# Optimization experiments

Hardware: AMD Instinct MI355X
Metric: run time of the kernel (lower is better)

## Reference

```python
import jax, jax.numpy as jnp
import numpy as np
from jax import lax

B, Q, T, G = 128, 900, 256, 20
FOCAL_ALPHA, FOCAL_GAMMA = 0.25, 2.0
COEF_BBOX, COEF_GIOU, COEF_CLASS = 5.0, 2.0, 1.0
EPS = 1e-6


def setup_inputs() -> dict:
    key = jax.random.key(0)
    k1, k2, k3, k4, k5 = jax.random.split(key, 5)
    pred_logits = jax.random.normal(k1, (B, Q, T), dtype=jnp.float32)
    # pred boxes in cxcywh, valid-ish: centers in (0.2,0.8), w/h in (0.05,0.3)
    cxy_p = jax.random.uniform(k2, (B, Q, 2), minval=0.2, maxval=0.8)
    wh_p = jax.random.uniform(k3, (B, Q, 2), minval=0.05, maxval=0.3)
    pred_boxes = jnp.concatenate([cxy_p, wh_p], axis=-1).astype(jnp.float32)
    cxy_t = jax.random.uniform(k4, (B, G, 2), minval=0.2, maxval=0.8)
    wh_t = jax.random.uniform(k5, (B, G, 2), minval=0.05, maxval=0.3)
    tgt_boxes = jnp.concatenate([cxy_t, wh_t], axis=-1).astype(jnp.float32)
    ks, kl = jax.random.split(jax.random.fold_in(key, 7))
    start = jax.random.randint(ks, (B, G, 1), 0, T - 6)
    length = jax.random.randint(kl, (B, G, 1), 1, 6)
    tokens_positive = jnp.concatenate([start, start + length], axis=-1).astype(jnp.int32)
    return {"pred_logits": pred_logits, "pred_boxes": pred_boxes,
            "tgt_boxes": tgt_boxes, "tokens_positive": tokens_positive}


def cxcywh_to_xyxy(b):
    cx, cy, w, h = b[..., 0], b[..., 1], b[..., 2], b[..., 3]
    return jnp.stack([cx - 0.5 * w, cy - 0.5 * h, cx + 0.5 * w, cy + 0.5 * h], axis=-1)


def box_iou_pairwise(b1, b2):
    # b1: [Q,4], b2: [G,4] xyxy -> iou [Q,G]
    a1 = (b1[:, 2] - b1[:, 0]) * (b1[:, 3] - b1[:, 1])
    a2 = (b2[:, 2] - b2[:, 0]) * (b2[:, 3] - b2[:, 1])
    lt = jnp.maximum(b1[:, None, :2], b2[None, :, :2])
    rb = jnp.minimum(b1[:, None, 2:], b2[None, :, 2:])
    wh = jnp.clip(rb - lt, 0.0)
    inter = wh[..., 0] * wh[..., 1]
    union = a1[:, None] + a2[None, :] - inter
    return inter / union


def giou_elementwise(b1, b2):
    # b1, b2: [G,4] xyxy (matched pairs) -> giou [G]
    a1 = (b1[:, 2] - b1[:, 0]) * (b1[:, 3] - b1[:, 1])
    a2 = (b2[:, 2] - b2[:, 0]) * (b2[:, 3] - b2[:, 1])
    lt = jnp.maximum(b1[:, :2], b2[:, :2])
    rb = jnp.minimum(b1[:, 2:], b2[:, 2:])
    wh = jnp.clip(rb - lt, 0.0)
    inter = wh[:, 0] * wh[:, 1]
    union = a1 + a2 - inter
    iou = inter / union
    lt_c = jnp.minimum(b1[:, :2], b2[:, :2])
    rb_c = jnp.maximum(b1[:, 2:], b2[:, 2:])
    wh_c = jnp.clip(rb_c - lt_c, 0.0)
    area_c = wh_c[:, 0] * wh_c[:, 1]
    return iou - (area_c - union) / area_c


def ensure_valid_boxes(b):
    x1, y1, x2, y2 = b[:, 0], b[:, 1], b[:, 2], b[:, 3]
    x2v = jnp.maximum(x2, x1 + EPS)
    y2v = jnp.maximum(y2, y1 + EPS)
    return jnp.clip(jnp.stack([x1, y1, x2v, y2v], axis=-1), 0.0, 1.0)


def sigmoid_focal_loss(logits, targets):
    p = jax.nn.sigmoid(logits)
    ce = jnp.maximum(logits, 0.0) - logits * targets + jnp.log1p(jnp.exp(-jnp.abs(logits)))
    p_t = p * targets + (1.0 - p) * (1.0 - targets)
    loss = ce * (1.0 - p_t) ** FOCAL_GAMMA
    alpha_t = FOCAL_ALPHA * targets + (1.0 - FOCAL_ALPHA) * (1.0 - targets)
    return (alpha_t * loss).mean()


def _per_batch(pred_boxes_b, pred_logits_b, tgt_boxes_b, spans_b):
    pred_xyxy = cxcywh_to_xyxy(pred_boxes_b)          # [Q,4]
    tgt_xyxy = cxcywh_to_xyxy(tgt_boxes_b)            # [G,4]
    iou = lax.stop_gradient(box_iou_pairwise(pred_xyxy, tgt_xyxy))  # [Q,G]

    # greedy sequential matching: for each gt column, argmax over remaining preds
    def step(mat, g):
        best = jnp.argmax(mat[:, g])
        mat = mat.at[best].set(-1.0)
        return mat, best
    _, matched = lax.scan(step, iou, jnp.arange(G))   # [G] pred indices

    matched_boxes = pred_boxes_b[matched]             # [G,4]
    loss_bbox = jnp.sum(jnp.abs(matched_boxes - tgt_boxes_b))

    matched_xyxy = ensure_valid_boxes(cxcywh_to_xyxy(matched_boxes))
    tgt_valid = ensure_valid_boxes(tgt_xyxy)
    giou = giou_elementwise(matched_xyxy, tgt_valid)
    loss_giou = jnp.sum(1.0 - giou)

    # target_classes [Q,T]: rows at matched indices get 1 over the gt token span
    pos = jnp.arange(T)
    span_mask = ((pos[None, :] >= spans_b[:, 0:1]) & (pos[None, :] < spans_b[:, 1:2])).astype(jnp.float32)  # [G,T]
    target_classes = jnp.zeros((Q, T), dtype=jnp.float32).at[matched].max(span_mask)

    loss_class = sigmoid_focal_loss(pred_logits_b, target_classes)
    return loss_bbox, loss_giou, loss_class


def reference(pred_logits, pred_boxes, tgt_boxes, tokens_positive):
    lb, lg, lc = jax.vmap(_per_batch)(pred_boxes, pred_logits, tgt_boxes, tokens_positive)
    num_boxes = jnp.float32(B * G)
    loss_bbox = COEF_BBOX * jnp.sum(lb) / num_boxes
    loss_giou = COEF_GIOU * jnp.sum(lg) / num_boxes
    loss_class = COEF_CLASS * jnp.sum(lc) / num_boxes
    loss_total = loss_bbox + loss_giou + loss_class
    return jnp.stack([loss_bbox, loss_giou, loss_class, loss_total])
```

## Files before the change

### kernel.cpp

```cpp
#include <hip/hip_runtime.h>
#include <hip/hip_bf16.h>

#define NB 128
#define NQ 900
#define NT 256
#define NG 20
#define NR 15
#define FOCAL_BLOCKS 1800
#define MATCH_BLOCKS 128
#define TOTAL_BLOCKS (FOCAL_BLOCKS + MATCH_BLOCKS)
#define FWAVES (FOCAL_BLOCKS * 4)

#define WS_BB 7200
#define WS_GI 7328
#define WS_DL 7456

__device__ __forceinline__ float clamp01(float v) {
    return fminf(fmaxf(v, 0.0f), 1.0f);
}

__device__ __forceinline__ float focal_neg_term(float x) {
    float ax  = fabsf(x);
    float em  = __expf(-ax);
    float a1  = 1.0f + em;
    float ce  = fmaxf(x, 0.0f) + __logf(a1);
    float inv = __builtin_amdgcn_rcpf(a1);
    float p   = (x >= 0.0f) ? inv : em * inv;
    return ce * p * p;
}

__device__ __forceinline__ float focal_delta_term(float x) {
    float ax     = fabsf(x);
    float em     = __expf(-ax);
    float a1     = 1.0f + em;
    float lg     = __logf(a1);
    float ce0    = fmaxf(x, 0.0f) + lg;
    float ce1    = ce0 - x;
    float inv    = __builtin_amdgcn_rcpf(a1);
    float em_inv = em * inv;
    float p      = (x >= 0.0f) ? inv : em_inv;
    float omp    = (x >= 0.0f) ? em_inv : inv;
    return 0.25f * ce1 * omp * omp - 0.75f * ce0 * p * p;
}

__device__ __forceinline__ float focal_row_sum4(float4 v) {
    return focal_neg_term(v.x) + focal_neg_term(v.y) +
           focal_neg_term(v.z) + focal_neg_term(v.w);
}

__global__ __launch_bounds__(256) void main_kernel(
    const float4* __restrict__ logits,
    const float4* __restrict__ pred_boxes,
    const float4* __restrict__ tgt_boxes,
    const int2*   __restrict__ tokens,
    float*        __restrict__ ws)
{
    if (blockIdx.x >= MATCH_BLOCKS) {
        const int lane = threadIdx.x & 63;
        const int gw   = ((blockIdx.x - MATCH_BLOCKS) * 256 + threadIdx.x) >> 6;

        float sum = 0.0f;
        #pragma unroll
        for (int i = 0; i < 2; ++i) {
            int row0 = (gw + i * FWAVES) * 8;
            const float4* base = logits + (size_t)row0 * (NT / 4) + lane;
            float4 v0 = base[0 * (NT / 4)];
            float4 v1 = base[1 * (NT / 4)];
            float4 v2 = base[2 * (NT / 4)];
            float4 v3 = base[3 * (NT / 4)];
            float4 v4 = base[4 * (NT / 4)];
            float4 v5 = base[5 * (NT / 4)];
            float4 v6 = base[6 * (NT / 4)];
            float4 v7 = base[7 * (NT / 4)];
            sum += focal_row_sum4(v0) + focal_row_sum4(v1) +
                   focal_row_sum4(v2) + focal_row_sum4(v3) +
                   focal_row_sum4(v4) + focal_row_sum4(v5) +
                   focal_row_sum4(v6) + focal_row_sum4(v7);
        }
        #pragma unroll
        for (int off = 32; off > 0; off >>= 1) sum += __shfl_down(sum, off);
        if (lane == 0) ws[gw] = sum;
        return;
    }

    if (threadIdx.x >= 64) return;
    const int b    = blockIdx.x;
    const int lane = threadIdx.x;

    float px1[NR], py1[NR], px2[NR], py2[NR], pa[NR];
    int avail = 0;
    #pragma unroll
    for (int r = 0; r < NR; ++r) {
        int q = lane + 64 * r;
        if (q < NQ) {
            float4 pb = pred_boxes[b * NQ + q];
            px1[r] = pb.x - 0.5f * pb.z; py1[r] = pb.y - 0.5f * pb.w;
            px2[r] = pb.x + 0.5f * pb.z; py2[r] = pb.y + 0.5f * pb.w;
            pa[r]  = (px2[r] - px1[r]) * (py2[r] - py1[r]);
            avail |= (1 << r);
        } else {
            px1[r] = 0.0f; py1[r] = 0.0f; px2[r] = 0.0f; py2[r] = 0.0f;
            pa[r] = 0.0f;
        }
    }

    int my_q = 0;
    for (int g = 0; g < NG; ++g) {
        float4 tb = tgt_boxes[b * NG + g];
        float gx1 = tb.x - 0.5f * tb.z, gy1 = tb.y - 0.5f * tb.w;
        float gx2 = tb.x + 0.5f * tb.z, gy2 = tb.y + 0.5f * tb.w;
        float ga  = (gx2 - gx1) * (gy2 - gy1);
        float bv = -2.0f;
        int   bi = 0x7fffffff;
        #pragma unroll
        for (int r = 0; r < NR; ++r) {
            float ix1 = fmaxf(px1[r], gx1), iy1 = fmaxf(py1[r], gy1);
            float ix2 = fminf(px2[r], gx2), iy2 = fminf(py2[r], gy2);
            float iw = fmaxf(ix2 - ix1, 0.0f), ih = fmaxf(iy2 - iy1, 0.0f);
            float inter = iw * ih;
            float v = inter / (pa[r] + ga - inter);
            bool ok = (avail >> r) & 1;
            v = ok ? v : -1.0f;
            int q = lane + 64 * r;
            if (v > bv) { bv = v; bi = q; }
        }
        #pragma unroll
        for (int off = 1; off < 64; off <<= 1) {
            float ov = __shfl_xor(bv, off);
            int   oi = __shfl_xor(bi, off);
            if (ov > bv || (ov == bv && oi < bi)) { bv = ov; bi = oi; }
        }
        if (lane == g) my_q = bi;
        if ((bi & 63) == lane) avail &= ~(1 << (bi >> 6));
    }

    float lb = 0.0f, lgi = 0.0f, dl = 0.0f;
    if (lane < NG) {
        int g = lane, q = my_q;
        float4 pb = pred_boxes[b * NQ + q];
        float4 tb = tgt_boxes[b * NG + g];
        lb = fabsf(pb.x - tb.x) + fabsf(pb.y - tb.y) +
             fabsf(pb.z - tb.z) + fabsf(pb.w - tb.w);

        float mx1 = pb.x - 0.5f * pb.z, my1 = pb.y - 0.5f * pb.w;
        float mx2 = pb.x + 0.5f * pb.z, my2 = pb.y + 0.5f * pb.w;
        mx2 = fmaxf(mx2, mx1 + 1e-6f);  my2 = fmaxf(my2, my1 + 1e-6f);
        mx1 = clamp01(mx1); my1 = clamp01(my1);
        mx2 = clamp01(mx2); my2 = clamp01(my2);

        float gx1 = tb.x - 0.5f * tb.z, gy1 = tb.y - 0.5f * tb.w;
        float gx2 = tb.x + 0.5f * tb.z, gy2 = tb.y + 0.5f * tb.w;
        gx2 = fmaxf(gx2, gx1 + 1e-6f);  gy2 = fmaxf(gy2, gy1 + 1e-6f);
        gx1 = clamp01(gx1); gy1 = clamp01(gy1);
        gx2 = clamp01(gx2); gy2 = clamp01(gy2);

        float a1 = (mx2 - mx1) * (my2 - my1);
        float a2 = (gx2 - gx1) * (gy2 - gy1);
        float ix1 = fmaxf(mx1, gx1), iy1 = fmaxf(my1, gy1);
        float ix2 = fminf(mx2, gx2), iy2 = fminf(my2, gy2);
        float iw = fmaxf(ix2 - ix1, 0.0f), ih = fmaxf(iy2 - iy1, 0.0f);
        float inter = iw * ih;
        float uni   = a1 + a2 - inter;
        float iou   = inter / uni;
        float cx1 = fminf(mx1, gx1), cy1 = fminf(my1, gy1);
        float cx2 = fmaxf(mx2, gx2), cy2 = fmaxf(my2, gy2);
        float ac  = fmaxf(cx2 - cx1, 0.0f) * fmaxf(cy2 - cy1, 0.0f);
        lgi = 1.0f - (iou - (ac - uni) / ac);

        int2 tk = tokens[b * NG + g];
        const float* rowp = (const float*)logits + (size_t)(b * NQ + q) * NT;
        for (int t = tk.x; t < tk.y; ++t) dl += focal_delta_term(rowp[t]);
    }
    #pragma unroll
    for (int off = 32; off > 0; off >>= 1) {
        lb  += __shfl_down(lb,  off);
        lgi += __shfl_down(lgi, off);
        dl  += __shfl_down(dl,  off);
    }
    if (lane == 0) {
        ws[WS_BB + b] = lb;
        ws[WS_GI + b] = lgi;
        ws[WS_DL + b] = dl;
    }
}

__global__ __launch_bounds__(256) void finalize_kernel(
    const float* __restrict__ ws, float* __restrict__ out)
{
    const int tid  = threadIdx.x;
    const int lane = tid & 63;
    const int wav  = tid >> 6;

    float s_neg = 0.0f;
    for (int i = tid; i < FWAVES; i += 256) s_neg += ws[i];
    float s_bb = 0.0f, s_gi = 0.0f, s_dl = 0.0f;
    if (tid < NB) {
        s_bb = ws[WS_BB + tid];
        s_gi = ws[WS_GI + tid];
        s_dl = ws[WS_DL + tid];
    }
    #pragma unroll
    for (int off = 32; off > 0; off >>= 1) {
        s_neg += __shfl_down(s_neg, off);
        s_bb  += __shfl_down(s_bb,  off);
        s_gi  += __shfl_down(s_gi,  off);
        s_dl  += __shfl_down(s_dl,  off);
    }
    __shared__ float red[4][4];
    if (lane == 0) {
        red[0][wav] = s_neg; red[1][wav] = s_bb;
        red[2][wav] = s_gi;  red[3][wav] = s_dl;
    }
    __syncthreads();
    if (tid == 0) {
        float neg = red[0][0] + red[0][1] + red[0][2] + red[0][3];
        float bb  = red[1][0] + red[1][1] + red[1][2] + red[1][3];
        float gi  = red[2][0] + red[2][1] + red[2][2] + red[2][3];
        float dlt = red[3][0] + red[3][1] + red[3][2] + red[3][3];
        const float num_boxes = (float)(NB * NG);
        float lb = 5.0f * bb / num_boxes;
        float lg = 2.0f * gi / num_boxes;
        float cls_sum = 0.75f * neg + dlt;
        float lc = (cls_sum / (float)(NQ * NT)) / num_boxes;
        out[0] = lb;
        out[1] = lg;
        out[2] = lc;
        out[3] = lb + lg + lc;
    }
}

extern "C" void kernel_launch(void* const* d_in, const int* in_sizes, int n_in,
                              void* d_out, int out_size, void* d_ws, size_t ws_size,
                              hipStream_t stream) {
    const float4* pred_logits4 = (const float4*)d_in[0];
    const float4* pred_boxes4  = (const float4*)d_in[1];
    const float4* tgt_boxes4   = (const float4*)d_in[2];
    const int2*   tokens2      = (const int2*)d_in[3];

    float* ws = (float*)d_ws;

    main_kernel<<<TOTAL_BLOCKS, 256, 0, stream>>>(pred_logits4, pred_boxes4,
                                                  tgt_boxes4, tokens2, ws);
    finalize_kernel<<<1, 256, 0, stream>>>(ws, (float*)d_out);
}
```

Before: 192.1 us.

## Fuse finalize into cooperative grid-synced kernel and shrink focal grid

Replaces the two-kernel launch with one cooperative kernel that does the partial work, a grid-wide sync, and the final reduction in block 0. The focal grid drops to 960 blocks so the grid can stay resident, and the focal loop becomes grid-stride. The matcher now stages pred boxes and areas in shared memory instead of 75 registers per lane. This removes the second launch and its gap, at the price of a grid barrier, fewer waves in flight for the memory-bound focal pass, and shared-memory reads in the matching inner loop. If the cooperative launch fails, it falls back to the old two-kernel path.

```diff
diff --git a/kernel.cpp b/kernel.cpp
--- a/kernel.cpp
+++ b/kernel.cpp
@@ -1,22 +1,33 @@
 #include <hip/hip_runtime.h>
 #include <hip/hip_bf16.h>
+#include <hip/hip_cooperative_groups.h>
+
+namespace cg = cooperative_groups;
 
 #define NB 128
 #define NQ 900
 #define NT 256
 #define NG 20
 #define NR 15
-#define FOCAL_BLOCKS 1800
+#define FOCAL_BLOCKS 832
 #define MATCH_BLOCKS 128
 #define TOTAL_BLOCKS (FOCAL_BLOCKS + MATCH_BLOCKS)
 #define FWAVES (FOCAL_BLOCKS * 4)
-
-#define WS_BB 7200
-#define WS_GI 7328
-#define WS_DL 7456
+#define NCHUNK 14400
+
+#define WS_BB 3328
+#define WS_GI 3456
+#define WS_DL 3584
 
 __device__ __forceinline__ float clamp01(float v) {
     return fminf(fmaxf(v, 0.0f), 1.0f);
+}
+
+__device__ __forceinline__ void ws_store(float* p, float v) {
+    __hip_atomic_store(p, v, __ATOMIC_RELAXED, __HIP_MEMORY_SCOPE_AGENT);
+}
+__device__ __forceinline__ float ws_load(const float* p) {
+    return __hip_atomic_load(p, __ATOMIC_RELAXED, __HIP_MEMORY_SCOPE_AGENT);
 }
 
 __device__ __forceinline__ float focal_neg_term(float x) {
@@ -48,61 +59,53 @@
            focal_neg_term(v.z) + focal_neg_term(v.w);
 }
 
-__global__ __launch_bounds__(256) void main_kernel(
-    const float4* __restrict__ logits,
-    const float4* __restrict__ pred_boxes,
-    const float4* __restrict__ tgt_boxes,
-    const int2*   __restrict__ tokens,
-    float*        __restrict__ ws)
-{
-    if (blockIdx.x >= MATCH_BLOCKS) {
-        const int lane = threadIdx.x & 63;
-        const int gw   = ((blockIdx.x - MATCH_BLOCKS) * 256 + threadIdx.x) >> 6;
-
-        float sum = 0.0f;
-        #pragma unroll
-        for (int i = 0; i < 2; ++i) {
-            int row0 = (gw + i * FWAVES) * 8;
-            const float4* base = logits + (size_t)row0 * (NT / 4) + lane;
-            float4 v0 = base[0 * (NT / 4)];
-            float4 v1 = base[1 * (NT / 4)];
-            float4 v2 = base[2 * (NT / 4)];
-            float4 v3 = base[3 * (NT / 4)];
-            float4 v4 = base[4 * (NT / 4)];
-            float4 v5 = base[5 * (NT / 4)];
-            float4 v6 = base[6 * (NT / 4)];
-            float4 v7 = base[7 * (NT / 4)];
-            sum += focal_row_sum4(v0) + focal_row_sum4(v1) +
-                   focal_row_sum4(v2) + focal_row_sum4(v3) +
-                   focal_row_sum4(v4) + focal_row_sum4(v5) +
-                   focal_row_sum4(v6) + focal_row_sum4(v7);
-        }
-        #pragma unroll
-        for (int off = 32; off > 0; off >>= 1) sum += __shfl_down(sum, off);
-        if (lane == 0) ws[gw] = sum;
-        return;
-    }
+__device__ void focal_path(const float4* __restrict__ logits,
+                           float* __restrict__ ws, int fblock) {
+    const int lane = threadIdx.x & 63;
+    const int gw   = (fblock * 256 + (int)threadIdx.x) >> 6;
+
+    float sum = 0.0f;
+    for (int c = gw; c < NCHUNK; c += FWAVES) {
+        const float4* base = logits + (size_t)(c * 8) * (NT / 4) + lane;
+        float4 v0 = base[0 * (NT / 4)];
+        float4 v1 = base[1 * (NT / 4)];
+        float4 v2 = base[2 * (NT / 4)];
+        float4 v3 = base[3 * (NT / 4)];
+        float4 v4 = base[4 * (NT / 4)];
+        float4 v5 = base[5 * (NT / 4)];
+        float4 v6 = base[6 * (NT / 4)];
+        float4 v7 = base[7 * (NT / 4)];
+        sum += focal_row_sum4(v0) + focal_row_sum4(v1) +
+               focal_row_sum4(v2) + focal_row_sum4(v3) +
+               focal_row_sum4(v4) + focal_row_sum4(v5) +
+               focal_row_sum4(v6) + focal_row_sum4(v7);
+    }
+    #pragma unroll
+    for (int off = 32; off > 0; off >>= 1) sum += __shfl_down(sum, off);
+    if (lane == 0) ws_store(&ws[gw], sum);
+}
+
+__device__ void match_path(const float4* __restrict__ logits,
+                           const float4* __restrict__ pred_boxes,
+                           const float4* __restrict__ tgt_boxes,
+                           const int2*   __restrict__ tokens,
+                           float* __restrict__ ws,
+                           float4* sbox, float* sarea, int b) {
+    for (int q = threadIdx.x; q < NQ; q += 256) {
+        float4 pb = pred_boxes[b * NQ + q];
+        float x1 = pb.x - 0.5f * pb.z, y1 = pb.y - 0.5f * pb.w;
+        float x2 = pb.x + 0.5f * pb.z, y2 = pb.y + 0.5f * pb.w;
+        sbox[q]  = make_float4(x1, y1, x2, y2);
+        sarea[q] = (x2 - x1) * (y2 - y1);
+    }
+    __syncthreads();
 
     if (threadIdx.x >= 64) return;
-    const int b    = blockIdx.x;
     const int lane = threadIdx.x;
-
-    float px1[NR], py1[NR], px2[NR], py2[NR], pa[NR];
-    int avail = 0;
+    int avail = (1 << NR) - 1;
     #pragma unroll
-    for (int r = 0; r < NR; ++r) {
-        int q = lane + 64 * r;
-        if (q < NQ) {
-            float4 pb = pred_boxes[b * NQ + q];
-            px1[r] = pb.x - 0.5f * pb.z; py1[r] = pb.y - 0.5f * pb.w;
-            px2[r] = pb.x + 0.5f * pb.z; py2[r] = pb.y + 0.5f * pb.w;
-            pa[r]  = (px2[r] - px1[r]) * (py2[r] - py1[r]);
-            avail |= (1 << r);
-        } else {
-            px1[r] = 0.0f; py1[r] = 0.0f; px2[r] = 0.0f; py2[r] = 0.0f;
-            pa[r] = 0.0f;
-        }
-    }
+    for (int r = 0; r < NR; ++r)
+        if (lane + 64 * r >= NQ) avail &= ~(1 << r);
 
     int my_q = 0;
     for (int g = 0; g < NG; ++g) {
@@ -114,14 +117,17 @@
         int   bi = 0x7fffffff;
         #pragma unroll
         for (int r = 0; r < NR; ++r) {
-            float ix1 = fmaxf(px1[r], gx1), iy1 = fmaxf(py1[r], gy1);
-            float ix2 = fminf(px2[r], gx2), iy2 = fminf(py2[r], gy2);
+            int q = lane + 64 * r;
+            bool ok = (avail >> r) & 1;
+            int qs = ok ? q : 0;
+            float4 pbx = sbox[qs];
+            float pa   = sarea[qs];
+            float ix1 = fmaxf(pbx.x, gx1), iy1 = fmaxf(pbx.y, gy1);
+            float ix2 = fminf(pbx.z, gx2), iy2 = fminf(pbx.w, gy2);
             float iw = fmaxf(ix2 - ix1, 0.0f), ih = fmaxf(iy2 - iy1, 0.0f);
             float inter = iw * ih;
-            float v = inter / (pa[r] + ga - inter);
-            bool ok = (avail >> r) & 1;
+            float v = inter / (pa + ga - inter);
             v = ok ? v : -1.0f;
-            int q = lane + 64 * r;
             if (v > bv) { bv = v; bi = q; }
         }
         #pragma unroll
@@ -178,26 +184,25 @@
         dl  += __shfl_down(dl,  off);
     }
     if (lane == 0) {
-        ws[WS_BB + b] = lb;
-        ws[WS_GI + b] = lgi;
-        ws[WS_DL + b] = dl;
-    }
-}
-
-__global__ __launch_bounds__(256) void finalize_kernel(
-    const float* __restrict__ ws, float* __restrict__ out)
-{
+        ws_store(&ws[WS_BB + b], lb);
+        ws_store(&ws[WS_GI + b], lgi);
+        ws_store(&ws[WS_DL + b], dl);
+    }
+}
+
+__device__ void finalize_body(const float* __restrict__ ws,
+                              float* __restrict__ out) {
     const int tid  = threadIdx.x;
     const int lane = tid & 63;
     const int wav  = tid >> 6;
 
     float s_neg = 0.0f;
-    for (int i = tid; i < FWAVES; i += 256) s_neg += ws[i];
+    for (int i = tid; i < FWAVES; i += 256) s_neg += ws_load(&ws[i]);
     float s_bb = 0.0f, s_gi = 0.0f, s_dl = 0.0f;
     if (tid < NB) {
-        s_bb = ws[WS_BB + tid];
-        s_gi = ws[WS_GI + tid];
-        s_dl = ws[WS_DL + tid];
+        s_bb = ws_load(&ws[WS_BB + tid]);
+        s_gi = ws_load(&ws[WS_GI + tid]);
+        s_dl = ws_load(&ws[WS_DL + tid]);
     }
     #pragma unroll
     for (int off = 32; off > 0; off >>= 1) {
@@ -229,6 +234,55 @@
     }
 }
 
+__global__ __launch_bounds__(256, 4) void coop_kernel(
+    const float4* __restrict__ logits,
+    const float4* __restrict__ pred_boxes,
+    const float4* __restrict__ tgt_boxes,
+    const int2*   __restrict__ tokens,
+    float*        __restrict__ ws,
+    float*        __restrict__ out)
+{
+    __shared__ float4 sbox[NQ];
+    __shared__ float  sarea[NQ];
+
+    if (blockIdx.x >= MATCH_BLOCKS) {
+        focal_path(logits, ws, blockIdx.x - MATCH_BLOCKS);
+    } else {
+        match_path(logits, pred_boxes, tgt_boxes, tokens, ws, sbox, sarea,
+                   blockIdx.x);
+    }
+
+    __threadfence();
+    cg::this_grid().sync();
+    __threadfence();
+
+    if (blockIdx.x == 0) finalize_body(ws, out);
+}
+
+__global__ __launch_bounds__(256, 4) void partials_kernel(
+    const float4* __restrict__ logits,
+    const float4* __restrict__ pred_boxes,
+    const float4* __restrict__ tgt_boxes,
+    const int2*   __restrict__ tokens,
+    float*        __restrict__ ws)
+{
+    __shared__ float4 sbox[NQ];
+    __shared__ float  sarea[NQ];
+
+    if (blockIdx.x >= MATCH_BLOCKS) {
+        focal_path(logits, ws, blockIdx.x - MATCH_BLOCKS);
+    } else {
+        match_path(logits, pred_boxes, tgt_boxes, tokens, ws, sbox, sarea,
+                   blockIdx.x);
+    }
+}
+
+__global__ __launch_bounds__(256) void finalize_kernel(
+    const float* __restrict__ ws, float* __restrict__ out)
+{
+    finalize_body(ws, out);
+}
+
 extern "C" void kernel_launch(void* const* d_in, const int* in_sizes, int n_in,
                               void* d_out, int out_size, void* d_ws, size_t ws_size,
                               hipStream_t stream) {
@@ -236,10 +290,19 @@
     const float4* pred_boxes4  = (const float4*)d_in[1];
     const float4* tgt_boxes4   = (const float4*)d_in[2];
     const int2*   tokens2      = (const int2*)d_in[3];
-
-    float* ws = (float*)d_ws;
-
-    main_kernel<<<TOTAL_BLOCKS, 256, 0, stream>>>(pred_logits4, pred_boxes4,
-                                                  tgt_boxes4, tokens2, ws);
-    finalize_kernel<<<1, 256, 0, stream>>>(ws, (float*)d_out);
-}
+    float*        ws           = (float*)d_ws;
+    float*        outp         = (float*)d_out;
+
+    void* args[] = { (void*)&pred_logits4, (void*)&pred_boxes4,
+                     (void*)&tgt_boxes4,   (void*)&tokens2,
+                     (void*)&ws,           (void*)&outp };
+    hipError_t err = hipLaunchCooperativeKernel((const void*)coop_kernel,
+                                                dim3(TOTAL_BLOCKS), dim3(256),
+                                                args, 0, stream);
+    if (err != hipSuccess) {
+        (void)hipGetLastError();
+        partials_kernel<<<TOTAL_BLOCKS, 256, 0, stream>>>(
+            pred_logits4, pred_boxes4, tgt_boxes4, tokens2, ws);
+        finalize_kernel<<<1, 256, 0, stream>>>(ws, outp);
+    }
+}
```

Measured after the change: 482.9 us. 151% more time.

## Fuse finalize reduction into main kernel via last-block ticket counter

Applied to the files above, without the earlier changes.

Removes the separate finalize launch. Each block now increments an atomic ticket in the workspace after its partial results. The block that sees the final count performs the global reduction and resets the ticket. The focal-loss loop also changes from two iterations of 8 rows to four iterations of 4 rows per wave, which alters load batching. The ticket logic assumes the workspace starts at a fixed poison value (0xAAAAAAAA), so correctness on the first call depends on how the harness initialises the workspace.

```diff
diff --git a/kernel.cpp b/kernel.cpp
--- a/kernel.cpp
+++ b/kernel.cpp
@@ -14,9 +14,18 @@
 #define WS_BB 7200
 #define WS_GI 7328
 #define WS_DL 7456
+#define WS_TICKET 7584
+#define TICKET_INIT 0xAAAAAAAAu
 
 __device__ __forceinline__ float clamp01(float v) {
     return fminf(fmaxf(v, 0.0f), 1.0f);
+}
+
+__device__ __forceinline__ void ws_store(float* p, float v) {
+    __hip_atomic_store(p, v, __ATOMIC_RELAXED, __HIP_MEMORY_SCOPE_AGENT);
+}
+__device__ __forceinline__ float ws_load(const float* p) {
+    return __hip_atomic_load(p, __ATOMIC_RELAXED, __HIP_MEMORY_SCOPE_AGENT);
 }
 
 __device__ __forceinline__ float focal_neg_term(float x) {
@@ -53,179 +62,186 @@
     const float4* __restrict__ pred_boxes,
     const float4* __restrict__ tgt_boxes,
     const int2*   __restrict__ tokens,
-    float*        __restrict__ ws)
+    float*        __restrict__ ws,
+    float*        __restrict__ out)
 {
     if (blockIdx.x >= MATCH_BLOCKS) {
         const int lane = threadIdx.x & 63;
-        const int gw   = ((blockIdx.x - MATCH_BLOCKS) * 256 + threadIdx.x) >> 6;
+        const int gw   = ((blockIdx.x - MATCH_BLOCKS) * 256 + (int)threadIdx.x) >> 6;
 
         float sum = 0.0f;
         #pragma unroll
-        for (int i = 0; i < 2; ++i) {
-            int row0 = (gw + i * FWAVES) * 8;
+        for (int i = 0; i < 4; ++i) {
+            int row0 = (gw + i * FWAVES) * 4;
             const float4* base = logits + (size_t)row0 * (NT / 4) + lane;
             float4 v0 = base[0 * (NT / 4)];
             float4 v1 = base[1 * (NT / 4)];
             float4 v2 = base[2 * (NT / 4)];
             float4 v3 = base[3 * (NT / 4)];
-            float4 v4 = base[4 * (NT / 4)];
-            float4 v5 = base[5 * (NT / 4)];
-            float4 v6 = base[6 * (NT / 4)];
-            float4 v7 = base[7 * (NT / 4)];
             sum += focal_row_sum4(v0) + focal_row_sum4(v1) +
-                   focal_row_sum4(v2) + focal_row_sum4(v3) +
-                   focal_row_sum4(v4) + focal_row_sum4(v5) +
-                   focal_row_sum4(v6) + focal_row_sum4(v7);
+                   focal_row_sum4(v2) + focal_row_sum4(v3);
         }
         #pragma unroll
         for (int off = 32; off > 0; off >>= 1) sum += __shfl_down(sum, off);
-        if (lane == 0) ws[gw] = sum;
-        return;
-    }
-
-    if (threadIdx.x >= 64) return;
-    const int b    = blockIdx.x;
-    const int lane = threadIdx.x;
-
-    float px1[NR], py1[NR], px2[NR], py2[NR], pa[NR];
-    int avail = 0;
-    #pragma unroll
-    for (int r = 0; r < NR; ++r) {
-        int q = lane + 64 * r;
-        if (q < NQ) {
+        if (lane == 0) ws_store(&ws[gw], sum);
+    } else if (threadIdx.x < 64) {
+        const int b    = blockIdx.x;
+        const int lane = threadIdx.x;
+
+        float px1[NR], py1[NR], px2[NR], py2[NR], pa[NR];
+        int avail = 0;
+        #pragma unroll
+        for (int r = 0; r < NR; ++r) {
+            int q = lane + 64 * r;
+            if (q < NQ) {
+                float4 pb = pred_boxes[b * NQ + q];
+                px1[r] = pb.x - 0.5f * pb.z; py1[r] = pb.y - 0.5f * pb.w;
+                px2[r] = pb.x + 0.5f * pb.z; py2[r] = pb.y + 0.5f * pb.w;
+                pa[r]  = (px2[r] - px1[r]) * (py2[r] - py1[r]);
+                avail |= (1 << r);
+            } else {
+                px1[r] = 0.0f; py1[r] = 0.0f; px2[r] = 0.0f; py2[r] = 0.0f;
+                pa[r] = 0.0f;
+            }
+        }
+
+        int my_q = 0;
+        for (int g = 0; g < NG; ++g) {
+            float4 tb = tgt_boxes[b * NG + g];
+            float gx1 = tb.x - 0.5f * tb.z, gy1 = tb.y - 0.5f * tb.w;
+            float gx2 = tb.x + 0.5f * tb.z, gy2 = tb.y + 0.5f * tb.w;
+            float ga  = (gx2 - gx1) * (gy2 - gy1);
+            float bv = -2.0f;
+            int   bi = 0x7fffffff;
+            #pragma unroll
+            for (int r = 0; r < NR; ++r) {
+                float ix1 = fmaxf(px1[r], gx1), iy1 = fmaxf(py1[r], gy1);
+                float ix2 = fminf(px2[r], gx2), iy2 = fminf(py2[r], gy2);
+                float iw = fmaxf(ix2 - ix1, 0.0f), ih = fmaxf(iy2 - iy1, 0.0f);
+                float inter = iw * ih;
+                float v = inter / (pa[r] + ga - inter);
+                bool ok = (avail >> r) & 1;
+                v = ok ? v : -1.0f;
+                int q = lane + 64 * r;
+                if (v > bv) { bv = v; bi = q; }
+            }
+            #pragma unroll
+            for (int off = 1; off < 64; off <<= 1) {
+                float ov = __shfl_xor(bv, off);
+                int   oi = __shfl_xor(bi, off);
+                if (ov > bv || (ov == bv && oi < bi)) { bv = ov; bi = oi; }
+            }
+            if (lane == g) my_q = bi;
+            if ((bi & 63) == lane) avail &= ~(1 << (bi >> 6));
+        }
+
+        float lb = 0.0f, lgi = 0.0f, dl = 0.0f;
+        if (lane < NG) {
+            int g = lane, q = my_q;
             float4 pb = pred_boxes[b * NQ + q];
-            px1[r] = pb.x - 0.5f * pb.z; py1[r] = pb.y - 0.5f * pb.w;
-            px2[r] = pb.x + 0.5f * pb.z; py2[r] = pb.y + 0.5f * pb.w;
-            pa[r]  = (px2[r] - px1[r]) * (py2[r] - py1[r]);
-            avail |= (1 << r);
-        } else {
-            px1[r] = 0.0f; py1[r] = 0.0f; px2[r] = 0.0f; py2[r] = 0.0f;
-            pa[r] = 0.0f;
-        }
-    }
-
-    int my_q = 0;
-    for (int g = 0; g < NG; ++g) {
-        float4 tb = tgt_boxes[b * NG + g];
-        float gx1 = tb.x - 0.5f * tb.z, gy1 = tb.y - 0.5f * tb.w;
-        float gx2 = tb.x + 0.5f * tb.z, gy2 = tb.y + 0.5f * tb.w;
-        float ga  = (gx2 - gx1) * (gy2 - gy1);
-        float bv = -2.0f;
-        int   bi = 0x7fffffff;
-        #pragma unroll
-        for (int r = 0; r < NR; ++r) {
-            float ix1 = fmaxf(px1[r], gx1), iy1 = fmaxf(py1[r], gy1);
-            float ix2 = fminf(px2[r], gx2), iy2 = fminf(py2[r], gy2);
+            float4 tb = tgt_boxes[b * NG + g];
+            lb = fabsf(pb.x - tb.x) + fabsf(pb.y - tb.y) +
+                 fabsf(pb.z - tb.z) + fabsf(pb.w - tb.w);
+
+            float mx1 = pb.x - 0.5f * pb.z, my1 = pb.y - 0.5f * pb.w;
+            float mx2 = pb.x + 0.5f * pb.z, my2 = pb.y + 0.5f * pb.w;
+            mx2 = fmaxf(mx2, mx1 + 1e-6f);  my2 = fmaxf(my2, my1 + 1e-6f);
+            mx1 = clamp01(mx1); my1 = clamp01(my1);
+            mx2 = clamp01(mx2); my2 = clamp01(my2);
+
+            float gx1 = tb.x - 0.5f * tb.z, gy1 = tb.y - 0.5f * tb.w;
+            float gx2 = tb.x + 0.5f * tb.z, gy2 = tb.y + 0.5f * tb.w;
+            gx2 = fmaxf(gx2, gx1 + 1e-6f);  gy2 = fmaxf(gy2, gy1 + 1e-6f);
+            gx1 = clamp01(gx1); gy1 = clamp01(gy1);
+            gx2 = clamp01(gx2); gy2 = clamp01(gy2);
+
+            float a1 = (mx2 - mx1) * (my2 - my1);
+            float a2 = (gx2 - gx1) * (gy2 - gy1);
+            float ix1 = fmaxf(mx1, gx1), iy1 = fmaxf(my1, gy1);
+            float ix2 = fminf(mx2, gx2), iy2 = fminf(my2, gy2);
             float iw = fmaxf(ix2 - ix1, 0.0f), ih = fmaxf(iy2 - iy1, 0.0f);
             float inter = iw * ih;
-            float v = inter / (pa[r] + ga - inter);
-            bool ok = (avail >> r) & 1;
-            v = ok ? v : -1.0f;
-            int q = lane + 64 * r;
-            if (v > bv) { bv = v; bi = q; }
-        }
-        #pragma unroll
-        for (int off = 1; off < 64; off <<= 1) {
-            float ov = __shfl_xor(bv, off);
-            int   oi = __shfl_xor(bi, off);
-            if (ov > bv || (ov == bv && oi < bi)) { bv = ov; bi = oi; }
-        }
-        if (lane == g) my_q = bi;
-        if ((bi & 63) == lane) avail &= ~(1 << (bi >> 6));
+            float uni   = a1 + a2 - inter;
+            float iou   = inter / uni;
+            float cx1 = fminf(mx1, gx1), cy1 = fminf(my1, gy1);
+            float cx2 = fmaxf(mx2, gx2), cy2 = fmaxf(my2, gy2);
+            float ac  = fmaxf(cx2 - cx1, 0.0f) * fmaxf(cy2 - cy1, 0.0f);
+            lgi = 1.0f - (iou - (ac - uni) / ac);
+
+            int2 tk = tokens[b * NG + g];
+            const float* rowp = (const float*)logits + (size_t)(b * NQ + q) * NT;
+            for (int t = tk.x; t < tk.y; ++t) dl += focal_delta_term(rowp[t]);
+        }
+        #pragma unroll
+        for (int off = 32; off > 0; off >>= 1) {
+            lb  += __shfl_down(lb,  off);
+            lgi += __shfl_down(lgi, off);
+            dl  += __shfl_down(dl,  off);
+        }
+        if (lane == 0) {
+            ws_store(&ws[WS_BB + b], lb);
+            ws_store(&ws[WS_GI + b], lgi);
+            ws_store(&ws[WS_DL + b], dl);
+        }
     }
 
-    float lb = 0.0f, lgi = 0.0f, dl = 0.0f;
-    if (lane < NG) {
-        int g = lane, q = my_q;
-        float4 pb = pred_boxes[b * NQ + q];
-        float4 tb = tgt_boxes[b * NG + g];
-        lb = fabsf(pb.x - tb.x) + fabsf(pb.y - tb.y) +
-             fabsf(pb.z - tb.z) + fabsf(pb.w - tb.w);
-
-        float mx1 = pb.x - 0.5f * pb.z, my1 = pb.y - 0.5f * pb.w;
-        float mx2 = pb.x + 0.5f * pb.z, my2 = pb.y + 0.5f * pb.w;
-        mx2 = fmaxf(mx2, mx1 + 1e-6f);  my2 = fmaxf(my2, my1 + 1e-6f);
-        mx1 = clamp01(mx1); my1 = clamp01(my1);
-        mx2 = clamp01(mx2); my2 = clamp01(my2);
-
-        float gx1 = tb.x - 0.5f * tb.z, gy1 = tb.y - 0.5f * tb.w;
-        float gx2 = tb.x + 0.5f * tb.z, gy2 = tb.y + 0.5f * tb.w;
-        gx2 = fmaxf(gx2, gx1 + 1e-6f);  gy2 = fmaxf(gy2, gy1 + 1e-6f);
-        gx1 = clamp01(gx1); gy1 = clamp01(gy1);
-        gx2 = clamp01(gx2); gy2 = clamp01(gy2);
-
-        float a1 = (mx2 - mx1) * (my2 - my1);
-        float a2 = (gx2 - gx1) * (gy2 - gy1);
-        float ix1 = fmaxf(mx1, gx1), iy1 = fmaxf(my1, gy1);
-        float ix2 = fminf(mx2, gx2), iy2 = fminf(my2, gy2);
-        float iw = fmaxf(ix2 - ix1, 0.0f), ih = fmaxf(iy2 - iy1, 0.0f);
-        float inter = iw * ih;
-        float uni   = a1 + a2 - inter;
-        float iou   = inter / uni;
-        float cx1 = fminf(mx1, gx1), cy1 = fminf(my1, gy1);
-        float cx2 = fmaxf(mx2, gx2), cy2 = fmaxf(my2, gy2);
-        float ac  = fmaxf(cx2 - cx1, 0.0f) * fmaxf(cy2 - cy1, 0.0f);
-        lgi = 1.0f - (iou - (ac - uni) / ac);
-
-        int2 tk = tokens[b * NG + g];
-        const float* rowp = (const float*)logits + (size_t)(b * NQ + q) * NT;
-        for (int t = tk.x; t < tk.y; ++t) dl += focal_delta_term(rowp[t]);
-    }
-    #pragma unroll
-    for (int off = 32; off > 0; off >>= 1) {
-        lb  += __shfl_down(lb,  off);
-        lgi += __shfl_down(lgi, off);
-        dl  += __shfl_down(dl,  off);
-    }
-    if (lane == 0) {
-        ws[WS_BB + b] = lb;
-        ws[WS_GI + b] = lgi;
-        ws[WS_DL + b] = dl;
-    }
-}
-
-__global__ __launch_bounds__(256) void finalize_kernel(
-    const float* __restrict__ ws, float* __restrict__ out)
-{
-    const int tid  = threadIdx.x;
-    const int lane = tid & 63;
-    const int wav  = tid >> 6;
-
-    float s_neg = 0.0f;
-    for (int i = tid; i < FWAVES; i += 256) s_neg += ws[i];
-    float s_bb = 0.0f, s_gi = 0.0f, s_dl = 0.0f;
-    if (tid < NB) {
-        s_bb = ws[WS_BB + tid];
-        s_gi = ws[WS_GI + tid];
-        s_dl = ws[WS_DL + tid];
-    }
-    #pragma unroll
-    for (int off = 32; off > 0; off >>= 1) {
-        s_neg += __shfl_down(s_neg, off);
-        s_bb  += __shfl_down(s_bb,  off);
-        s_gi  += __shfl_down(s_gi,  off);
-        s_dl  += __shfl_down(s_dl,  off);
-    }
-    __shared__ float red[4][4];
-    if (lane == 0) {
-        red[0][wav] = s_neg; red[1][wav] = s_bb;
-        red[2][wav] = s_gi;  red[3][wav] = s_dl;
+    __shared__ bool lastFlag;
+    unsigned int* ticket = (unsigned int*)&ws[WS_TICKET];
+
+    __threadfence();
+    __syncthreads();
+    if (threadIdx.x == 0) {
+        unsigned int old = __hip_atomic_fetch_add(
+            ticket, 1u, __ATOMIC_ACQ_REL, __HIP_MEMORY_SCOPE_AGENT);
+        lastFlag = (old == TICKET_INIT + (unsigned)(TOTAL_BLOCKS - 1));
     }
     __syncthreads();
-    if (tid == 0) {
-        float neg = red[0][0] + red[0][1] + red[0][2] + red[0][3];
-        float bb  = red[1][0] + red[1][1] + red[1][2] + red[1][3];
-        float gi  = red[2][0] + red[2][1] + red[2][2] + red[2][3];
-        float dlt = red[3][0] + red[3][1] + red[3][2] + red[3][3];
-        const float num_boxes = (float)(NB * NG);
-        float lb = 5.0f * bb / num_boxes;
-        float lg = 2.0f * gi / num_boxes;
-        float cls_sum = 0.75f * neg + dlt;
-        float lc = (cls_sum / (float)(NQ * NT)) / num_boxes;
-        out[0] = lb;
-        out[1] = lg;
-        out[2] = lc;
-        out[3] = lb + lg + lc;
+    if (!lastFlag) return;
+
+    __threadfence();
+    {
+        const int tid  = threadIdx.x;
+        const int lane = tid & 63;
+        const int wav  = tid >> 6;
+
+        float s_neg = 0.0f;
+        for (int i = tid; i < FWAVES; i += 256) s_neg += ws_load(&ws[i]);
+        float s_bb = 0.0f, s_gi = 0.0f, s_dl = 0.0f;
+        if (tid < NB) {
+            s_bb = ws_load(&ws[WS_BB + tid]);
+            s_gi = ws_load(&ws[WS_GI + tid]);
+            s_dl = ws_load(&ws[WS_DL + tid]);
+        }
+        #pragma unroll
+        for (int off = 32; off > 0; off >>= 1) {
+            s_neg += __shfl_down(s_neg, off);
+            s_bb  += __shfl_down(s_bb,  off);
+            s_gi  += __shfl_down(s_gi,  off);
+            s_dl  += __shfl_down(s_dl,  off);
+        }
+        __shared__ float red[4][4];
+        if (lane == 0) {
+            red[0][wav] = s_neg; red[1][wav] = s_bb;
+            red[2][wav] = s_gi;  red[3][wav] = s_dl;
+        }
+        __syncthreads();
+        if (tid == 0) {
+            float neg = red[0][0] + red[0][1] + red[0][2] + red[0][3];
+            float bb  = red[1][0] + red[1][1] + red[1][2] + red[1][3];
+            float gi  = red[2][0] + red[2][1] + red[2][2] + red[2][3];
+            float dlt = red[3][0] + red[3][1] + red[3][2] + red[3][3];
+            const float num_boxes = (float)(NB * NG);
+            float lbo = 5.0f * bb / num_boxes;
+            float lgo = 2.0f * gi / num_boxes;
+            float cls_sum = 0.75f * neg + dlt;
+            float lco = (cls_sum / (float)(NQ * NT)) / num_boxes;
+            out[0] = lbo;
+            out[1] = lgo;
+            out[2] = lco;
+            out[3] = lbo + lgo + lco;
+            __hip_atomic_store(ticket, TICKET_INIT, __ATOMIC_RELAXED,
+                               __HIP_MEMORY_SCOPE_AGENT);
+        }
     }
 }
 
@@ -236,10 +252,9 @@
     const float4* pred_boxes4  = (const float4*)d_in[1];
     const float4* tgt_boxes4   = (const float4*)d_in[2];
     const int2*   tokens2      = (const int2*)d_in[3];
-
-    float* ws = (float*)d_ws;
+    float*        ws           = (float*)d_ws;
+    float*        outp         = (float*)d_out;
 
     main_kernel<<<TOTAL_BLOCKS, 256, 0, stream>>>(pred_logits4, pred_boxes4,
-                                                  tgt_boxes4, tokens2, ws);
-    finalize_kernel<<<1, 256, 0, stream>>>(ws, (float*)d_out);
-}
+                                                  tgt_boxes4, tokens2, ws, outp);
+}
```

Measured after the change: 479.1 us. +149.4%, slower.
